# Performance work log

Measured on AMD Instinct MI355X. Metric: run time of the kernel, lower is better.

The kernel has to match this reference:

```python
import jax, jax.numpy as jnp
import numpy as np

DIM = 1152
N_HEADS = 12
GROUPS = 6
KV_HEADS = N_HEADS // GROUPS  # 2
HEAD_DIM = DIM // N_HEADS     # 96
BASE = 10000.0
BSZ = 4
SEQ = 2048
MAX_SEQ = 2048
NEG_INF = -1e9


def rope(x, start_pos):
    # x: [b, s, h, d]; interleaved (even/odd) rotary embedding, matching the torch code
    b, s, h, d = x.shape
    x_even = x[..., 0::2]
    x_odd = x[..., 1::2]
    # even positions <- -x_odd, odd positions <- x_even (interleaved)
    x_rev = jnp.stack([-x_odd, x_even], axis=-1).reshape(x.shape)
    i = jnp.repeat(jnp.arange(0, d, 2), 2).astype(x.dtype)  # [d]
    theta = 1.0 / (BASE ** (i / d))                          # [d]
    pos = jnp.arange(start_pos + s, dtype=x.dtype)           # [s] (start_pos=0 case, as in source)
    ang = pos[:, None] * theta[None, :]                      # [s, d]
    cos = jnp.cos(ang).reshape(1, s, 1, d)
    sin = jnp.sin(ang).reshape(1, s, 1, d)
    return x * cos + x_rev * sin


def setup_inputs() -> dict:
    key = jax.random.key(0)
    ks = jax.random.split(key, 4)
    sc = 0.02
    x = jax.random.normal(ks[0], (BSZ, SEQ, DIM), jnp.float32)
    # causal mask [S, end_pos]: 0 on/below diagonal, large negative above
    mask = jnp.triu(jnp.full((SEQ, SEQ), NEG_INF, jnp.float32), k=1)
    q_w = jax.random.normal(ks[1], (DIM, DIM), jnp.float32) * sc
    q_b = jnp.zeros((DIM,), jnp.float32)
    kv_w = jax.random.normal(ks[2], (2 * KV_HEADS * HEAD_DIM, DIM), jnp.float32) * sc
    kv_b = jnp.zeros((2 * KV_HEADS * HEAD_DIM,), jnp.float32)
    wo_w = jax.random.normal(ks[3], (DIM, DIM), jnp.float32) * sc
    wo_b = jnp.zeros((DIM,), jnp.float32)
    return {"x": x, "mask": mask, "q_w": q_w, "q_b": q_b, "kv_w": kv_w,
            "kv_b": kv_b, "wo_w": wo_w, "wo_b": wo_b, "start_pos": 0}


def reference(x, mask, q_w, q_b, kv_w, kv_b, wo_w, wo_b, start_pos):
    b, s, f = x.shape
    end = start_pos + s
    q = (x @ q_w.T + q_b).reshape(b, s, N_HEADS, HEAD_DIM)
    kv = (x @ kv_w.T + kv_b).reshape(b, s, 2, KV_HEADS, HEAD_DIM)
    k, v = kv[:, :, 0], kv[:, :, 1]
    rq = rope(q, start_pos)
    rk = rope(k, start_pos)
    # KV-cache write (cache initialized to zeros, as in the buffer)
    k_cache = jnp.zeros((b, MAX_SEQ, KV_HEADS, HEAD_DIM), x.dtype).at[:, start_pos:end].set(rk)
    v_cache = jnp.zeros((b, MAX_SEQ, KV_HEADS, HEAD_DIM), x.dtype).at[:, start_pos:end].set(v)
    # repeat_kv: head index = kv_head * groups + g  -> jnp.repeat along head axis
    kk = jnp.repeat(k_cache[:, :end], GROUPS, axis=2)  # [b, t, H, d]
    vv = jnp.repeat(v_cache[:, :end], GROUPS, axis=2)
    scale = HEAD_DIM ** -0.5
    attn = jnp.einsum('bshd,bthd->bsht', rq, kk) * scale
    attn = attn + mask[:, None, :]  # mask [s, t] -> [s, 1, t] broadcast over b, h
    scores = jax.nn.softmax(attn.astype(jnp.float32), axis=-1).astype(x.dtype)
    out = jnp.einsum('bsht,bthd->bshd', scores, vv).reshape(b, s, DIM)
    return out @ wo_w.T + wo_b
```

## Files before the change

### kernel.cpp

```cpp
#include <hip/hip_runtime.h>
#include <hip/hip_bf16.h>

constexpr int DIMD  = 1152;
constexpr int NHD   = 12;
constexpr int KVHD  = 2;
constexpr int HDD   = 96;
constexpr int GRPS  = 6;
constexpr int SEQL  = 2048;
constexpr int BSZ4  = 4;
constexpr int MROWS = BSZ4 * SEQL;
constexpr int NQKV  = DIMD + 2 * KVHD * HDD;
constexpr float SCALE = 0.10206207261596577f;

typedef short  bf16x8 __attribute__((ext_vector_type(8)));
typedef float  f32x4  __attribute__((ext_vector_type(4)));

typedef __attribute__((address_space(3))) unsigned int       lds_u32_t;
typedef __attribute__((address_space(1))) const unsigned int glb_u32_t;

__device__ __forceinline__ void gload16(const unsigned short* g, unsigned short* l) {
    __builtin_amdgcn_global_load_lds((glb_u32_t*)(const void*)g,
                                     (lds_u32_t*)(void*)l, 16, 0, 0);
}

__device__ __forceinline__ unsigned short f2bf(float f) {
    unsigned int u = __builtin_bit_cast(unsigned int, f);
    u += 0x7fff + ((u >> 16) & 1);
    return (unsigned short)(u >> 16);
}

__global__ __launch_bounds__(256) void cvt_bf16_kernel(
    const float4* __restrict__ src, ushort4* __restrict__ dst, int n4)
{
    int i = blockIdx.x * 256 + threadIdx.x;
    if (i < n4) {
        float4 f = src[i];
        ushort4 o;
        o.x = f2bf(f.x); o.y = f2bf(f.y); o.z = f2bf(f.z); o.w = f2bf(f.w);
        dst[i] = o;
    }
}

__global__ __launch_bounds__(256) void rope_tab_kernel(
    const int* __restrict__ start_pos, float2* __restrict__ tab)
{
    int i = blockIdx.x * 256 + threadIdx.x;
    if (i < SEQL * 48) {
        int s = i / 48, j = i - (i / 48) * 48;
        float th = powf(10000.0f, -(float)(2 * j) / 96.0f);
        float ang = (float)(s + *start_pos) * th;
        float sn, cs; sincosf(ang, &sn, &cs);
        tab[i] = make_float2(cs, sn);
    }
}

__global__ __launch_bounds__(256) void qkv_mfma_kernel(
    const unsigned short* __restrict__ xb,  const unsigned short* __restrict__ qwb,
    const unsigned short* __restrict__ kvwb,
    const float* __restrict__ qb,  const float* __restrict__ kvb,
    const float2* __restrict__ tab,
    unsigned short* __restrict__ Qo, unsigned short* __restrict__ Ko,
    unsigned short* __restrict__ VTo)
{
    __shared__ __align__(16) unsigned short As[2][128 * 32];
    __shared__ __align__(16) unsigned short Bs[2][128 * 32];

    const int tid  = threadIdx.x;
    const int w    = tid >> 6;
    const int lane = tid & 63;
    const int l16  = lane & 15;
    const int quad = lane >> 4;
    const int wm   = w >> 1, wn = w & 1;
    const int m0   = blockIdx.y * 128;
    const int n0   = blockIdx.x * 128;

    const unsigned short* Abase = xb + (size_t)m0 * DIMD;
    const unsigned short* Bbase = (n0 < DIMD)
        ? qwb  + (size_t)n0 * DIMD
        : kvwb + (size_t)(n0 - DIMD) * DIMD;

    const int srow = w * 16 + (lane >> 2);
    const int scol = (lane & 3) * 8;

    f32x4 acc[4][4];
    #pragma unroll
    for (int mi = 0; mi < 4; mi++)
        #pragma unroll
        for (int ni = 0; ni < 4; ni++) acc[mi][ni] = (f32x4){0.f, 0.f, 0.f, 0.f};

    constexpr int NK = DIMD / 32;

    gload16(Abase + (size_t)srow        * DIMD + scol, &As[0][w * 512]);
    gload16(Abase + (size_t)(srow + 64) * DIMD + scol, &As[0][2048 + w * 512]);
    gload16(Bbase + (size_t)srow        * DIMD + scol, &Bs[0][w * 512]);
    gload16(Bbase + (size_t)(srow + 64) * DIMD + scol, &Bs[0][2048 + w * 512]);

    for (int kt = 0; kt < NK; kt++) {
        const int cur = kt & 1;
        if (kt + 1 < NK) {
            const int k0 = (kt + 1) * 32;
            gload16(Abase + (size_t)srow        * DIMD + k0 + scol, &As[cur ^ 1][w * 512]);
            gload16(Abase + (size_t)(srow + 64) * DIMD + k0 + scol, &As[cur ^ 1][2048 + w * 512]);
            gload16(Bbase + (size_t)srow        * DIMD + k0 + scol, &Bs[cur ^ 1][w * 512]);
            gload16(Bbase + (size_t)(srow + 64) * DIMD + k0 + scol, &Bs[cur ^ 1][2048 + w * 512]);
            asm volatile("s_waitcnt vmcnt(4)" ::: "memory");
        } else {
            asm volatile("s_waitcnt vmcnt(0)" ::: "memory");
        }
        __builtin_amdgcn_s_barrier();
        asm volatile("" ::: "memory");

        bf16x8 af[4], bfr[4];
        #pragma unroll
        for (int mi = 0; mi < 4; mi++)
            af[mi] = *(const bf16x8*)&As[cur][(wm * 64 + mi * 16 + l16) * 32 + quad * 8];
        #pragma unroll
        for (int ni = 0; ni < 4; ni++)
            bfr[ni] = *(const bf16x8*)&Bs[cur][(wn * 64 + ni * 16 + l16) * 32 + quad * 8];
        #pragma unroll
        for (int mi = 0; mi < 4; mi++)
            #pragma unroll
            for (int ni = 0; ni < 4; ni++)
                acc[mi][ni] = __builtin_amdgcn_mfma_f32_16x16x32_bf16(
                    af[mi], bfr[ni], acc[mi][ni], 0, 0, 0);

        asm volatile("" ::: "memory");
        __builtin_amdgcn_s_barrier();
    }

    #pragma unroll
    for (int ni = 0; ni < 4; ni++) {
        const int n   = n0 + wn * 64 + ni * 16 + l16;
        const bool isQ = (n < DIMD);
        const int jj  = n - DIMD;
        const bool isK = !isQ && (jj < KVHD * HDD);
        const int d   = isQ ? (n % HDD) : (jj % HDD);
        const int hh  = isQ ? (n / HDD) : ((jj / HDD) & 1);
        const float bias = isQ ? qb[n] : kvb[jj];
        const bool doRope = isQ || isK;
        const int de2 = (d >> 1);
        const float sg = (n & 1) ? 1.0f : -1.0f;
        #pragma unroll
        for (int mi = 0; mi < 4; mi++) {
            #pragma unroll
            for (int r = 0; r < 4; r++) {
                const int m = m0 + wm * 64 + mi * 16 + quad * 4 + r;
                const int b = m >> 11;
                const int s = m & (SEQL - 1);
                float v  = acc[mi][ni][r] + bias;
                float pv = __shfl_xor(v, 1, 64);
                float o = v;
                if (doRope) {
                    float2 cs2 = tab[s * 48 + de2];
                    o = v * cs2.x + sg * pv * cs2.y;
                }
                if (isQ)
                    Qo[(((size_t)b * NHD + hh) * SEQL + s) * HDD + d] = f2bf(o);
                else if (isK)
                    Ko[(((size_t)b * KVHD + hh) * SEQL + s) * HDD + d] = f2bf(o);
                else
                    VTo[(((size_t)b * KVHD + hh) * HDD + d) * SEQL + s] = f2bf(o);
            }
        }
    }
}

__global__ __launch_bounds__(256, 3) void attn_mfma_kernel(
    const unsigned short* __restrict__ Q, const unsigned short* __restrict__ K,
    const unsigned short* __restrict__ VT, unsigned short* __restrict__ AO)
{
    constexpr int KHALF = 64 * 104;
    __shared__ __align__(16) unsigned short Ks[2 * KHALF];
    __shared__ __align__(16) unsigned short VTs[96 * 72];
    __shared__ __align__(16) unsigned short Ps[4][16 * 72];
    __shared__ float Al[4][16];

    const int tid  = threadIdx.x;
    const int w    = tid >> 6;
    const int lane = tid & 63;
    const int l16  = lane & 15;
    const int quad = lane >> 4;

    const int idx = (int)blockIdx.x;
    const int qi  = idx / 48;
    const int hb  = idx - qi * 48;
    const int qt  = 31 - qi;
    const int h   = hb % NHD;
    const int b   = hb / NHD;
    const int kvh = h / GRPS;
    const int nkb = qt + 1;

    const unsigned short* Qbase  = Q  + (((size_t)b * NHD  + h)   * SEQL) * HDD;
    const unsigned short* Kbase  = K  + (((size_t)b * KVHD + kvh) * SEQL) * HDD;
    const unsigned short* VTbase = VT + (((size_t)b * KVHD + kvh) * HDD)  * SEQL;

    int goff[7]; int gkind[7]; int loff[7];
    #pragma unroll
    for (int j = 0; j < 7; j++) {
        const int i = w + 4 * j;
        gkind[j] = 2; goff[j] = 0; loff[j] = 0;
        if (i < 13) {
            int slot = i * 64 + lane;
            int r = slot / 13, g = slot - r * 13;
            goff[j]  = r * HDD + (g < 12 ? g * 8 : 0);
            gkind[j] = 0;
            loff[j]  = i * 512;
        } else if (i < 27) {
            int iv = i - 13;
            int slot = iv * 64 + lane;
            if (slot < 864) {
                int r = slot / 9, g = slot - r * 9;
                goff[j]  = r * SEQL + (g < 8 ? g * 8 : 0);
                gkind[j] = 1;
                loff[j]  = iv * 512;
            }
        }
    }

    bf16x8 qf[3];
    {
        const int qrow = qt * 64 + w * 16 + l16;
        const unsigned short* qp = Qbase + (size_t)qrow * HDD + quad * 8;
        qf[0] = *(const bf16x8*)(qp);
        qf[1] = *(const bf16x8*)(qp + 32);
        qf[2] = *(const bf16x8*)(qp + 64);
    }

    float m_r = -1e30f, l_r = 0.0f;
    f32x4 oacc[6];
    #pragma unroll
    for (int nn = 0; nn < 6; nn++) oacc[nn] = (f32x4){0.f, 0.f, 0.f, 0.f};

    #pragma unroll
    for (int j = 0; j < 7; j++)
        if (gkind[j] == 0)
            gload16(Kbase + goff[j], &Ks[loff[j]]);
    #pragma unroll
    for (int j = 0; j < 7; j++)
        if (gkind[j] == 1) {
            if ((w + 4 * j) < 26 || lane < 32)
                gload16(VTbase + goff[j], &VTs[loff[j]]);
        }

    const int dql = w * 16 + l16;

    for (int kb = 0; kb < nkb; kb++) {
        const int  cur  = kb & 1;
        const bool more = (kb + 1 < nkb);

        if (more) {
            const size_t kg = (size_t)(kb + 1) * 64 * HDD;
            #pragma unroll
            for (int j = 0; j < 7; j++)
                if (gkind[j] == 0)
                    gload16(Kbase + kg + goff[j], &Ks[(cur ^ 1) * KHALF + loff[j]]);
            asm volatile("s_waitcnt vmcnt(6)" ::: "memory");
        } else {
            asm volatile("s_waitcnt vmcnt(3)" ::: "memory");
        }
        __builtin_amdgcn_s_barrier();
        asm volatile("" ::: "memory");

        const unsigned short* ksb = &Ks[cur * KHALF];
        f32x4 s[4];
        __builtin_amdgcn_s_setprio(1);
        #pragma unroll
        for (int n = 0; n < 4; n++) {
            const unsigned short* kr = ksb + (n * 16 + l16) * 104 + quad * 8;
            bf16x8 kf0 = *(const bf16x8*)(kr);
            bf16x8 kf1 = *(const bf16x8*)(kr + 32);
            bf16x8 kf2 = *(const bf16x8*)(kr + 64);
            f32x4 a = (f32x4){0.f, 0.f, 0.f, 0.f};
            a = __builtin_amdgcn_mfma_f32_16x16x32_bf16(kf0, qf[0], a, 0, 0, 0);
            a = __builtin_amdgcn_mfma_f32_16x16x32_bf16(kf1, qf[1], a, 0, 0, 0);
            a = __builtin_amdgcn_mfma_f32_16x16x32_bf16(kf2, qf[2], a, 0, 0, 0);
            s[n] = a;
        }
        __builtin_amdgcn_s_setprio(0);

        float v[4][4];
        float mx = -3e30f;
        if (!more) {
            #pragma unroll
            for (int n = 0; n < 4; n++)
                #pragma unroll
                for (int r = 0; r < 4; r++) {
                    float x = s[n][r] * SCALE;
                    if (n * 16 + quad * 4 + r > dql) x = -1e30f;
                    v[n][r] = x;
                    mx = fmaxf(mx, x);
                }
        } else {
            #pragma unroll
            for (int n = 0; n < 4; n++)
                #pragma unroll
                for (int r = 0; r < 4; r++) {
                    float x = s[n][r] * SCALE;
                    v[n][r] = x;
                    mx = fmaxf(mx, x);
                }
        }
        mx = fmaxf(mx, __shfl_xor(mx, 16, 64));
        mx = fmaxf(mx, __shfl_xor(mx, 32, 64));
        const float mnew = fmaxf(m_r, mx);
        const float al = __expf(m_r - mnew);
        if (quad == 0) Al[w][l16] = al;
        float sum = 0.0f;
        #pragma unroll
        for (int n = 0; n < 4; n++) {
            float p0 = __expf(v[n][0] - mnew);
            float p1 = __expf(v[n][1] - mnew);
            float p2 = __expf(v[n][2] - mnew);
            float p3 = __expf(v[n][3] - mnew);
            sum += (p0 + p1) + (p2 + p3);
            ushort4 pk;
            pk.x = f2bf(p0); pk.y = f2bf(p1); pk.z = f2bf(p2); pk.w = f2bf(p3);
            *(ushort4*)&Ps[w][l16 * 72 + n * 16 + quad * 4] = pk;
        }
        sum += __shfl_xor(sum, 16, 64);
        sum += __shfl_xor(sum, 32, 64);
        l_r = l_r * al + sum;
        m_r = mnew;
        __builtin_amdgcn_wave_barrier();

        const float4 alb = *(const float4*)&Al[w][quad * 4];
        bf16x8 pa0 = *(const bf16x8*)&Ps[w][l16 * 72 + quad * 8];
        bf16x8 pa1 = *(const bf16x8*)&Ps[w][l16 * 72 + 32 + quad * 8];
        const float albr[4] = {alb.x, alb.y, alb.z, alb.w};

        if (more) asm volatile("s_waitcnt vmcnt(3)" ::: "memory");
        else      asm volatile("s_waitcnt vmcnt(0)" ::: "memory");
        __builtin_amdgcn_s_barrier();
        asm volatile("" ::: "memory");

        __builtin_amdgcn_s_setprio(1);
        #pragma unroll
        for (int nn = 0; nn < 6; nn++) {
            const unsigned short* vr = &VTs[(nn * 16 + l16) * 72 + quad * 8];
            bf16x8 vb0 = *(const bf16x8*)(vr);
            bf16x8 vb1 = *(const bf16x8*)(vr + 32);
            f32x4 a = oacc[nn];
            #pragma unroll
            for (int r = 0; r < 4; r++) a[r] *= albr[r];
            a = __builtin_amdgcn_mfma_f32_16x16x32_bf16(pa0, vb0, a, 0, 0, 0);
            a = __builtin_amdgcn_mfma_f32_16x16x32_bf16(pa1, vb1, a, 0, 0, 0);
            oacc[nn] = a;
        }
        __builtin_amdgcn_s_setprio(0);

        asm volatile("" ::: "memory");
        __builtin_amdgcn_s_barrier();
        asm volatile("" ::: "memory");

        if (more) {
            const int kg = (kb + 1) * 64;
            #pragma unroll
            for (int j = 0; j < 7; j++)
                if (gkind[j] == 1) {
                    if ((w + 4 * j) < 26 || lane < 32)
                        gload16(VTbase + kg + goff[j], &VTs[loff[j]]);
                }
        }
    }

    const float linv = 1.0f / l_r;
    if (quad == 0) Al[w][l16] = linv;
    __builtin_amdgcn_wave_barrier();
    const float4 lb4 = *(const float4*)&Al[w][quad * 4];
    const float lbr[4] = {lb4.x, lb4.y, lb4.z, lb4.w};
    const int row0 = qt * 64 + w * 16 + quad * 4;
    #pragma unroll
    for (int nn = 0; nn < 6; nn++) {
        #pragma unroll
        for (int r = 0; r < 4; r++) {
            AO[((size_t)b * SEQL + row0 + r) * DIMD + h * HDD + nn * 16 + l16] =
                f2bf(oacc[nn][r] * lbr[r]);
        }
    }
}

__global__ __launch_bounds__(256) void out_mfma_kernel(
    const unsigned short* __restrict__ Ab, const unsigned short* __restrict__ Wb,
    const float* __restrict__ wob, float* __restrict__ out)
{
    __shared__ __align__(16) unsigned short As[2][128 * 32];
    __shared__ __align__(16) unsigned short Bs[2][128 * 32];

    const int tid  = threadIdx.x;
    const int w    = tid >> 6;
    const int lane = tid & 63;
    const int l16  = lane & 15;
    const int quad = lane >> 4;
    const int wm   = w >> 1, wn = w & 1;
    const int m0   = blockIdx.y * 128;
    const int n0   = blockIdx.x * 128;

    const unsigned short* Abase = Ab + (size_t)m0 * DIMD;
    const unsigned short* Bbase = Wb + (size_t)n0 * DIMD;

    const int srow = w * 16 + (lane >> 2);
    const int scol = (lane & 3) * 8;

    f32x4 acc[4][4];
    #pragma unroll
    for (int mi = 0; mi < 4; mi++)
        #pragma unroll
        for (int ni = 0; ni < 4; ni++) acc[mi][ni] = (f32x4){0.f, 0.f, 0.f, 0.f};

    constexpr int NK = DIMD / 32;

    gload16(Abase + (size_t)srow        * DIMD + scol, &As[0][w * 512]);
    gload16(Abase + (size_t)(srow + 64) * DIMD + scol, &As[0][2048 + w * 512]);
    gload16(Bbase + (size_t)srow        * DIMD + scol, &Bs[0][w * 512]);
    gload16(Bbase + (size_t)(srow + 64) * DIMD + scol, &Bs[0][2048 + w * 512]);

    for (int kt = 0; kt < NK; kt++) {
        const int cur = kt & 1;
        if (kt + 1 < NK) {
            const int k0 = (kt + 1) * 32;
            gload16(Abase + (size_t)srow        * DIMD + k0 + scol, &As[cur ^ 1][w * 512]);
            gload16(Abase + (size_t)(srow + 64) * DIMD + k0 + scol, &As[cur ^ 1][2048 + w * 512]);
            gload16(Bbase + (size_t)srow        * DIMD + k0 + scol, &Bs[cur ^ 1][w * 512]);
            gload16(Bbase + (size_t)(srow + 64) * DIMD + k0 + scol, &Bs[cur ^ 1][2048 + w * 512]);
            asm volatile("s_waitcnt vmcnt(4)" ::: "memory");
        } else {
            asm volatile("s_waitcnt vmcnt(0)" ::: "memory");
        }
        __builtin_amdgcn_s_barrier();
        asm volatile("" ::: "memory");

        bf16x8 af[4], bfr[4];
        #pragma unroll
        for (int mi = 0; mi < 4; mi++)
            af[mi] = *(const bf16x8*)&As[cur][(wm * 64 + mi * 16 + l16) * 32 + quad * 8];
        #pragma unroll
        for (int ni = 0; ni < 4; ni++)
            bfr[ni] = *(const bf16x8*)&Bs[cur][(wn * 64 + ni * 16 + l16) * 32 + quad * 8];
        #pragma unroll
        for (int mi = 0; mi < 4; mi++)
            #pragma unroll
            for (int ni = 0; ni < 4; ni++)
                acc[mi][ni] = __builtin_amdgcn_mfma_f32_16x16x32_bf16(
                    af[mi], bfr[ni], acc[mi][ni], 0, 0, 0);

        asm volatile("" ::: "memory");
        __builtin_amdgcn_s_barrier();
    }

    #pragma unroll
    for (int ni = 0; ni < 4; ni++) {
        const int n = n0 + wn * 64 + ni * 16 + l16;
        const float bias = wob[n];
        #pragma unroll
        for (int mi = 0; mi < 4; mi++) {
            #pragma unroll
            for (int r = 0; r < 4; r++) {
                const int m = m0 + wm * 64 + mi * 16 + quad * 4 + r;
                out[(size_t)m * DIMD + n] = acc[mi][ni][r] + bias;
            }
        }
    }
}

extern "C" void kernel_launch(void* const* d_in, const int* in_sizes, int n_in,
                              void* d_out, int out_size, void* d_ws, size_t ws_size,
                              hipStream_t stream)
{
    const float* x   = (const float*)d_in[0];
    const float* qw  = (const float*)d_in[2];
    const float* qb  = (const float*)d_in[3];
    const float* kvw = (const float*)d_in[4];
    const float* kvb = (const float*)d_in[5];
    const float* wow = (const float*)d_in[6];
    const float* wob = (const float*)d_in[7];
    const int*   sp  = (const int*)d_in[8];

    const size_t xN   = (size_t)MROWS * DIMD;
    const size_t qwN  = (size_t)DIMD * DIMD;
    const size_t kvwN = (size_t)2 * KVHD * HDD * DIMD;
    const size_t qN   = (size_t)BSZ4 * NHD  * SEQL * HDD;
    const size_t kvN  = (size_t)BSZ4 * KVHD * SEQL * HDD;

    unsigned short* xb   = (unsigned short*)d_ws;
    unsigned short* qwb  = xb   + xN;
    unsigned short* kvwb = qwb  + qwN;
    unsigned short* wowb = kvwb + kvwN;
    unsigned short* Q16  = wowb + qwN;
    unsigned short* K16  = Q16  + qN;
    unsigned short* VT16 = K16  + kvN;
    unsigned short* AO16 = VT16 + kvN;
    float2* tab = (float2*)AO16;

    cvt_bf16_kernel<<<(int)(xN / 4 + 255) / 256, 256, 0, stream>>>(
        (const float4*)x, (ushort4*)xb, (int)(xN / 4));
    cvt_bf16_kernel<<<(int)(qwN / 4 + 255) / 256, 256, 0, stream>>>(
        (const float4*)qw, (ushort4*)qwb, (int)(qwN / 4));
    cvt_bf16_kernel<<<(int)(kvwN / 4 + 255) / 256, 256, 0, stream>>>(
        (const float4*)kvw, (ushort4*)kvwb, (int)(kvwN / 4));
    cvt_bf16_kernel<<<(int)(qwN / 4 + 255) / 256, 256, 0, stream>>>(
        (const float4*)wow, (ushort4*)wowb, (int)(qwN / 4));
    rope_tab_kernel<<<(SEQL * 48 + 255) / 256, 256, 0, stream>>>(sp, tab);

    qkv_mfma_kernel<<<dim3(NQKV / 128, MROWS / 128, 1), 256, 0, stream>>>(
        xb, qwb, kvwb, qb, kvb, tab, Q16, K16, VT16);
    attn_mfma_kernel<<<dim3((SEQL / 64) * NHD * BSZ4, 1, 1), 256, 0, stream>>>(
        Q16, K16, VT16, AO16);
    out_mfma_kernel<<<dim3(DIMD / 128, MROWS / 128, 1), 256, 0, stream>>>(
        AO16, wowb, wob, (float*)d_out);
}
```

Before: 309.6 us.

## Switch attention to 32x32 MFMA with 128-row query tiles and register P

Rewrites the flash-attention kernel to use 32x32x16 bf16 MFMA, with each wave owning 32 query rows and each block 128 rows. The probability tile is packed to bf16 with v_cvt_pk and redistributed between half-waves by shuffles, so the LDS round trip for P goes away. Waves whose rows are fully masked skip compute, and blocks are ordered to interleave long and short causal tiles. The changes aim to cut LDS traffic and raise MFMA efficiency, at the cost of more registers (occupancy hint lowered to 2) and fewer, larger blocks.

```diff
diff --git a/kernel.cpp b/kernel.cpp
--- a/kernel.cpp
+++ b/kernel.cpp
@@ -14,6 +14,8 @@
 
 typedef short  bf16x8 __attribute__((ext_vector_type(8)));
 typedef float  f32x4  __attribute__((ext_vector_type(4)));
+typedef float  f32x16 __attribute__((ext_vector_type(16)));
+typedef unsigned int u32x4_t __attribute__((ext_vector_type(4)));
 
 typedef __attribute__((address_space(3))) unsigned int       lds_u32_t;
 typedef __attribute__((address_space(1))) const unsigned int glb_u32_t;
@@ -27,6 +29,12 @@
     unsigned int u = __builtin_bit_cast(unsigned int, f);
     u += 0x7fff + ((u >> 16) & 1);
     return (unsigned short)(u >> 16);
+}
+
+__device__ __forceinline__ unsigned cvtpk(float a, float b) {
+    unsigned r;
+    asm volatile("v_cvt_pk_bf16_f32 %0, %1, %2" : "=v"(r) : "v"(a), "v"(b));
+    return r;
 }
 
 __global__ __launch_bounds__(256) void cvt_bf16_kernel(
@@ -165,30 +173,29 @@
     }
 }
 
-__global__ __launch_bounds__(256, 3) void attn_mfma_kernel(
+__global__ __launch_bounds__(256, 2) void attn_mfma_kernel(
     const unsigned short* __restrict__ Q, const unsigned short* __restrict__ K,
     const unsigned short* __restrict__ VT, unsigned short* __restrict__ AO)
 {
     constexpr int KHALF = 64 * 104;
     __shared__ __align__(16) unsigned short Ks[2 * KHALF];
     __shared__ __align__(16) unsigned short VTs[96 * 72];
-    __shared__ __align__(16) unsigned short Ps[4][16 * 72];
-    __shared__ float Al[4][16];
+    __shared__ float Al[4][32];
 
     const int tid  = threadIdx.x;
     const int w    = tid >> 6;
     const int lane = tid & 63;
-    const int l16  = lane & 15;
-    const int quad = lane >> 4;
+    const int l31  = lane & 31;
+    const int hi   = lane >> 5;
 
     const int idx = (int)blockIdx.x;
-    const int qi  = idx / 48;
-    const int hb  = idx - qi * 48;
-    const int qt  = 31 - qi;
+    const int ord = idx / 48;
+    const int hb  = idx - ord * 48;
+    const int qt  = (ord < 8) ? (15 - 2 * ord) : (2 * ord - 16);
     const int h   = hb % NHD;
     const int b   = hb / NHD;
     const int kvh = h / GRPS;
-    const int nkb = qt + 1;
+    const int nkb = 2 * qt + 2;
 
     const unsigned short* Qbase  = Q  + (((size_t)b * NHD  + h)   * SEQL) * HDD;
     const unsigned short* Kbase  = K  + (((size_t)b * KVHD + kvh) * SEQL) * HDD;
@@ -217,19 +224,21 @@
         }
     }
 
-    bf16x8 qf[3];
+    const int qv   = qt * 128 + w * 32;
+    const int qabs = qv + l31;
+    bf16x8 qf[6];
     {
-        const int qrow = qt * 64 + w * 16 + l16;
-        const unsigned short* qp = Qbase + (size_t)qrow * HDD + quad * 8;
-        qf[0] = *(const bf16x8*)(qp);
-        qf[1] = *(const bf16x8*)(qp + 32);
-        qf[2] = *(const bf16x8*)(qp + 64);
+        const unsigned short* qp = Qbase + (size_t)(qv + l31) * HDD + hi * 8;
+        #pragma unroll
+        for (int ks = 0; ks < 6; ks++) qf[ks] = *(const bf16x8*)(qp + ks * 16);
     }
 
     float m_r = -1e30f, l_r = 0.0f;
-    f32x4 oacc[6];
-    #pragma unroll
-    for (int nn = 0; nn < 6; nn++) oacc[nn] = (f32x4){0.f, 0.f, 0.f, 0.f};
+    f32x16 oacc[3];
+    #pragma unroll
+    for (int nn = 0; nn < 3; nn++)
+        #pragma unroll
+        for (int r = 0; r < 16; r++) oacc[nn][r] = 0.0f;
 
     #pragma unroll
     for (int j = 0; j < 7; j++)
@@ -242,11 +251,11 @@
                 gload16(VTbase + goff[j], &VTs[loff[j]]);
         }
 
-    const int dql = w * 16 + l16;
-
     for (int kb = 0; kb < nkb; kb++) {
         const int  cur  = kb & 1;
         const bool more = (kb + 1 < nkb);
+        const int  k0   = kb * 64;
+        const bool active = (k0 <= qv + 31);
 
         if (more) {
             const size_t kg = (size_t)(kb + 1) * 64 * HDD;
@@ -261,92 +270,112 @@
         __builtin_amdgcn_s_barrier();
         asm volatile("" ::: "memory");
 
-        const unsigned short* ksb = &Ks[cur * KHALF];
-        f32x4 s[4];
-        __builtin_amdgcn_s_setprio(1);
-        #pragma unroll
-        for (int n = 0; n < 4; n++) {
-            const unsigned short* kr = ksb + (n * 16 + l16) * 104 + quad * 8;
-            bf16x8 kf0 = *(const bf16x8*)(kr);
-            bf16x8 kf1 = *(const bf16x8*)(kr + 32);
-            bf16x8 kf2 = *(const bf16x8*)(kr + 64);
-            f32x4 a = (f32x4){0.f, 0.f, 0.f, 0.f};
-            a = __builtin_amdgcn_mfma_f32_16x16x32_bf16(kf0, qf[0], a, 0, 0, 0);
-            a = __builtin_amdgcn_mfma_f32_16x16x32_bf16(kf1, qf[1], a, 0, 0, 0);
-            a = __builtin_amdgcn_mfma_f32_16x16x32_bf16(kf2, qf[2], a, 0, 0, 0);
-            s[n] = a;
-        }
-        __builtin_amdgcn_s_setprio(0);
-
-        float v[4][4];
-        float mx = -3e30f;
-        if (!more) {
-            #pragma unroll
-            for (int n = 0; n < 4; n++)
-                #pragma unroll
-                for (int r = 0; r < 4; r++) {
-                    float x = s[n][r] * SCALE;
-                    if (n * 16 + quad * 4 + r > dql) x = -1e30f;
-                    v[n][r] = x;
-                    mx = fmaxf(mx, x);
+        bf16x8 pa[4];
+        float  albr[16];
+
+        if (active) {
+            const unsigned short* ksb = &Ks[cur * KHALF];
+            f32x16 s0, s1;
+            #pragma unroll
+            for (int r = 0; r < 16; r++) { s0[r] = 0.0f; s1[r] = 0.0f; }
+            __builtin_amdgcn_s_setprio(1);
+            #pragma unroll
+            for (int ks = 0; ks < 6; ks++) {
+                bf16x8 kf0 = *(const bf16x8*)&ksb[l31 * 104        + ks * 16 + hi * 8];
+                bf16x8 kf1 = *(const bf16x8*)&ksb[(32 + l31) * 104 + ks * 16 + hi * 8];
+                s0 = __builtin_amdgcn_mfma_f32_32x32x16_bf16(kf0, qf[ks], s0, 0, 0, 0);
+                s1 = __builtin_amdgcn_mfma_f32_32x32x16_bf16(kf1, qf[ks], s1, 0, 0, 0);
+            }
+            __builtin_amdgcn_s_setprio(0);
+
+            float p0[16], p1[16];
+            float mx = -3e30f;
+            const bool domask = (k0 + 63 > qv);
+            #pragma unroll
+            for (int r = 0; r < 16; r++) {
+                const int tl = (r & 3) + 8 * (r >> 2) + 4 * hi;
+                float x0 = s0[r] * SCALE;
+                float x1 = s1[r] * SCALE;
+                if (domask) {
+                    if (k0 + tl      > qabs) x0 = -1e30f;
+                    if (k0 + 32 + tl > qabs) x1 = -1e30f;
                 }
-        } else {
-            #pragma unroll
-            for (int n = 0; n < 4; n++)
-                #pragma unroll
-                for (int r = 0; r < 4; r++) {
-                    float x = s[n][r] * SCALE;
-                    v[n][r] = x;
-                    mx = fmaxf(mx, x);
+                p0[r] = x0; p1[r] = x1;
+                mx = fmaxf(mx, fmaxf(x0, x1));
+            }
+            mx = fmaxf(mx, __shfl_xor(mx, 32, 64));
+            const float mnew = fmaxf(m_r, mx);
+            const float al = __expf(m_r - mnew);
+            if (hi == 0) Al[w][l31] = al;
+            float sum = 0.0f;
+            #pragma unroll
+            for (int r = 0; r < 16; r++) {
+                p0[r] = __expf(p0[r] - mnew);
+                p1[r] = __expf(p1[r] - mnew);
+                sum += p0[r] + p1[r];
+            }
+            sum += __shfl_xor(sum, 32, 64);
+            l_r = l_r * al + sum;
+            m_r = mnew;
+
+            #pragma unroll
+            for (int ks = 0; ks < 4; ks++) {
+                const int base = (ks & 1) * 8;
+                unsigned pkA0, pkA1, pkB0, pkB1;
+                if (ks < 2) {
+                    pkA0 = cvtpk(p0[base + 0], p0[base + 1]);
+                    pkA1 = cvtpk(p0[base + 2], p0[base + 3]);
+                    pkB0 = cvtpk(p0[base + 4], p0[base + 5]);
+                    pkB1 = cvtpk(p0[base + 6], p0[base + 7]);
+                } else {
+                    pkA0 = cvtpk(p1[base + 0], p1[base + 1]);
+                    pkA1 = cvtpk(p1[base + 2], p1[base + 3]);
+                    pkB0 = cvtpk(p1[base + 4], p1[base + 5]);
+                    pkB1 = cvtpk(p1[base + 6], p1[base + 7]);
                 }
-        }
-        mx = fmaxf(mx, __shfl_xor(mx, 16, 64));
-        mx = fmaxf(mx, __shfl_xor(mx, 32, 64));
-        const float mnew = fmaxf(m_r, mx);
-        const float al = __expf(m_r - mnew);
-        if (quad == 0) Al[w][l16] = al;
-        float sum = 0.0f;
-        #pragma unroll
-        for (int n = 0; n < 4; n++) {
-            float p0 = __expf(v[n][0] - mnew);
-            float p1 = __expf(v[n][1] - mnew);
-            float p2 = __expf(v[n][2] - mnew);
-            float p3 = __expf(v[n][3] - mnew);
-            sum += (p0 + p1) + (p2 + p3);
-            ushort4 pk;
-            pk.x = f2bf(p0); pk.y = f2bf(p1); pk.z = f2bf(p2); pk.w = f2bf(p3);
-            *(ushort4*)&Ps[w][l16 * 72 + n * 16 + quad * 4] = pk;
-        }
-        sum += __shfl_xor(sum, 16, 64);
-        sum += __shfl_xor(sum, 32, 64);
-        l_r = l_r * al + sum;
-        m_r = mnew;
-        __builtin_amdgcn_wave_barrier();
-
-        const float4 alb = *(const float4*)&Al[w][quad * 4];
-        bf16x8 pa0 = *(const bf16x8*)&Ps[w][l16 * 72 + quad * 8];
-        bf16x8 pa1 = *(const bf16x8*)&Ps[w][l16 * 72 + 32 + quad * 8];
-        const float albr[4] = {alb.x, alb.y, alb.z, alb.w};
+                unsigned S0 = hi ? pkA0 : pkB0;
+                unsigned S1 = hi ? pkA1 : pkB1;
+                unsigned R0 = __shfl_xor(S0, 32, 64);
+                unsigned R1 = __shfl_xor(S1, 32, 64);
+                u32x4_t wv;
+                wv[0] = hi ? R0 : pkA0;
+                wv[1] = hi ? R1 : pkA1;
+                wv[2] = hi ? pkB0 : R0;
+                wv[3] = hi ? pkB1 : R1;
+                pa[ks] = __builtin_bit_cast(bf16x8, wv);
+            }
+            __builtin_amdgcn_wave_barrier();
+            const float4 a0 = *(const float4*)&Al[w][hi * 4];
+            const float4 a1 = *(const float4*)&Al[w][8 + hi * 4];
+            const float4 a2 = *(const float4*)&Al[w][16 + hi * 4];
+            const float4 a3 = *(const float4*)&Al[w][24 + hi * 4];
+            albr[0] = a0.x; albr[1] = a0.y; albr[2]  = a0.z; albr[3]  = a0.w;
+            albr[4] = a1.x; albr[5] = a1.y; albr[6]  = a1.z; albr[7]  = a1.w;
+            albr[8] = a2.x; albr[9] = a2.y; albr[10] = a2.z; albr[11] = a2.w;
+            albr[12] = a3.x; albr[13] = a3.y; albr[14] = a3.z; albr[15] = a3.w;
+        }
 
         if (more) asm volatile("s_waitcnt vmcnt(3)" ::: "memory");
         else      asm volatile("s_waitcnt vmcnt(0)" ::: "memory");
         __builtin_amdgcn_s_barrier();
         asm volatile("" ::: "memory");
 
-        __builtin_amdgcn_s_setprio(1);
-        #pragma unroll
-        for (int nn = 0; nn < 6; nn++) {
-            const unsigned short* vr = &VTs[(nn * 16 + l16) * 72 + quad * 8];
-            bf16x8 vb0 = *(const bf16x8*)(vr);
-            bf16x8 vb1 = *(const bf16x8*)(vr + 32);
-            f32x4 a = oacc[nn];
-            #pragma unroll
-            for (int r = 0; r < 4; r++) a[r] *= albr[r];
-            a = __builtin_amdgcn_mfma_f32_16x16x32_bf16(pa0, vb0, a, 0, 0, 0);
-            a = __builtin_amdgcn_mfma_f32_16x16x32_bf16(pa1, vb1, a, 0, 0, 0);
-            oacc[nn] = a;
-        }
-        __builtin_amdgcn_s_setprio(0);
+        if (active) {
+            __builtin_amdgcn_s_setprio(1);
+            #pragma unroll
+            for (int nn = 0; nn < 3; nn++) {
+                f32x16 a = oacc[nn];
+                #pragma unroll
+                for (int r = 0; r < 16; r++) a[r] *= albr[r];
+                #pragma unroll
+                for (int tk = 0; tk < 4; tk++) {
+                    bf16x8 vb = *(const bf16x8*)&VTs[(nn * 32 + l31) * 72 + tk * 16 + hi * 8];
+                    a = __builtin_amdgcn_mfma_f32_32x32x16_bf16(pa[tk], vb, a, 0, 0, 0);
+                }
+                oacc[nn] = a;
+            }
+            __builtin_amdgcn_s_setprio(0);
+        }
 
         asm volatile("" ::: "memory");
         __builtin_amdgcn_s_barrier();
@@ -364,16 +393,25 @@
     }
 
     const float linv = 1.0f / l_r;
-    if (quad == 0) Al[w][l16] = linv;
+    if (hi == 0) Al[w][l31] = linv;
     __builtin_amdgcn_wave_barrier();
-    const float4 lb4 = *(const float4*)&Al[w][quad * 4];
-    const float lbr[4] = {lb4.x, lb4.y, lb4.z, lb4.w};
-    const int row0 = qt * 64 + w * 16 + quad * 4;
-    #pragma unroll
-    for (int nn = 0; nn < 6; nn++) {
-        #pragma unroll
-        for (int r = 0; r < 4; r++) {
-            AO[((size_t)b * SEQL + row0 + r) * DIMD + h * HDD + nn * 16 + l16] =
+    float lbr[16];
+    {
+        const float4 a0 = *(const float4*)&Al[w][hi * 4];
+        const float4 a1 = *(const float4*)&Al[w][8 + hi * 4];
+        const float4 a2 = *(const float4*)&Al[w][16 + hi * 4];
+        const float4 a3 = *(const float4*)&Al[w][24 + hi * 4];
+        lbr[0] = a0.x; lbr[1] = a0.y; lbr[2]  = a0.z; lbr[3]  = a0.w;
+        lbr[4] = a1.x; lbr[5] = a1.y; lbr[6]  = a1.z; lbr[7]  = a1.w;
+        lbr[8] = a2.x; lbr[9] = a2.y; lbr[10] = a2.z; lbr[11] = a2.w;
+        lbr[12] = a3.x; lbr[13] = a3.y; lbr[14] = a3.z; lbr[15] = a3.w;
+    }
+    #pragma unroll
+    for (int nn = 0; nn < 3; nn++) {
+        #pragma unroll
+        for (int r = 0; r < 16; r++) {
+            const int tl = (r & 3) + 8 * (r >> 2) + 4 * hi;
+            AO[((size_t)b * SEQL + qv + tl) * DIMD + h * HDD + nn * 32 + l31] =
                 f2bf(oacc[nn][r] * lbr[r]);
         }
     }
@@ -503,7 +541,7 @@
 
     qkv_mfma_kernel<<<dim3(NQKV / 128, MROWS / 128, 1), 256, 0, stream>>>(
         xb, qwb, kvwb, qb, kvb, tab, Q16, K16, VT16);
-    attn_mfma_kernel<<<dim3((SEQL / 64) * NHD * BSZ4, 1, 1), 256, 0, stream>>>(
+    attn_mfma_kernel<<<dim3(16 * 48, 1, 1), 256, 0, stream>>>(
         Q16, K16, VT16, AO16);
     out_mfma_kernel<<<dim3(DIMD / 128, MROWS / 128, 1), 256, 0, stream>>>(
         AO16, wowb, wob, (float*)d_out);
```

After: 345.2 us. +11.5%, slower.
